# Kernel tuning notes

Measured on AMD Instinct MI355X. Metric: run time of the kernel, lower is better.

The kernel has to match this reference:

```python
import jax, jax.numpy as jnp
import numpy as np
from jax import lax

B, L, NCH, NQ, NL, FW, NCLS = 256, 3000, 4, 8, 2, 128, 5
BN_EPS = 1e-5


def setup_inputs() -> dict:
    key = jax.random.key(0)
    ks = jax.random.split(key, 24)
    rn = lambda k, shape, s=0.05: jax.random.normal(k, shape, jnp.float32) * s
    inp = {}
    inp['x'] = jax.random.normal(ks[0], (B, NCH, L), jnp.float32)
    inp['conv1_w'] = rn(ks[1], (32, NCH, 7)); inp['conv1_b'] = rn(ks[2], (32,))
    inp['bn1_g'] = 1.0 + rn(ks[3], (32,)); inp['bn1_b'] = rn(ks[3], (32,))
    inp['conv2_w'] = rn(ks[4], (64, 32, 7)); inp['conv2_b'] = rn(ks[5], (64,))
    inp['bn2_g'] = 1.0 + rn(ks[6], (64,)); inp['bn2_b'] = rn(ks[6], (64,))
    inp['conv3_w'] = rn(ks[7], (128, 64, 7)); inp['conv3_b'] = rn(ks[8], (128,))
    inp['bn3_g'] = 1.0 + rn(ks[9], (128,)); inp['bn3_b'] = rn(ks[9], (128,))
    inp['conv4_w'] = rn(ks[10], (128, 128, 7)); inp['conv4_b'] = rn(ks[11], (128,))
    inp['bn4_g'] = 1.0 + rn(ks[12], (128,)); inp['bn4_b'] = rn(ks[12], (128,))
    inp['fc_w'] = rn(ks[13], (FW, 128)); inp['fc_b'] = rn(ks[14], (FW,))
    inp['ang_w'] = rn(ks[15], (NQ, FW)); inp['ang_b'] = rn(ks[16], (NQ,))
    # TorchLayer default init: uniform in [0, 2*pi)
    inp['qw'] = jax.random.uniform(ks[17], (NL, NQ, 3), jnp.float32, 0.0, 2.0 * np.pi)
    inp['h1_w'] = rn(ks[18], (64, NQ)); inp['h1_b'] = rn(ks[19], (64,))
    inp['h2_w'] = rn(ks[20], (NCLS, 64)); inp['h2_b'] = rn(ks[21], (NCLS,))
    return inp


def _conv1d(x, w, b):
    y = lax.conv_general_dilated(x, w, (1,), [(3, 3)], dimension_numbers=('NCH', 'OIH', 'NCH'))
    return y + b[None, :, None]


def _bn(x, g, b):  # eval-mode BN: running_mean=0, running_var=1
    inv = 1.0 / np.sqrt(1.0 + BN_EPS)
    return x * (g * inv)[None, :, None] + b[None, :, None]


def _maxpool4(x):
    return lax.reduce_window(x, -jnp.inf, lax.max, (1, 1, 4), (1, 1, 4), 'VALID')


def _apply_1q(state, U, w, batched):
    # state: (B, 2**NQ); wire 0 = most significant bit (PennyLane convention)
    bs = state.shape[0]
    st = state.reshape(bs, 2 ** w, 2, -1)
    if batched:
        new = jnp.einsum('sab,slbr->slar', U, st)
    else:
        new = jnp.einsum('ab,slbr->slar', U, st)
    return new.reshape(bs, -1)


def _apply_cnot(state, c, t):
    bs = state.shape[0]
    q1, q2 = min(c, t), max(c, t)
    s = state.reshape(bs, 2 ** q1, 2, 2 ** (q2 - q1 - 1), 2, -1)
    ci, ti = (2, 4) if c < t else (4, 2)
    c0 = lax.index_in_dim(s, 0, ci, keepdims=True)
    c1 = jnp.flip(lax.index_in_dim(s, 1, ci, keepdims=True), axis=ti)
    return jnp.concatenate([c0, c1], axis=ci).reshape(bs, -1)


def _rot_matrix(phi, th, om):
    # PennyLane Rot(phi, theta, omega) = RZ(omega) RY(theta) RZ(phi)
    cm, sm = jnp.cos(th / 2), jnp.sin(th / 2)
    m00 = jnp.exp(-0.5j * (phi + om)) * cm
    m01 = -jnp.exp(0.5j * (phi - om)) * sm
    m10 = jnp.exp(-0.5j * (phi - om)) * sm
    m11 = jnp.exp(0.5j * (phi + om)) * cm
    return jnp.stack([jnp.stack([m00, m01]), jnp.stack([m10, m11])]).astype(jnp.complex64)


def _qsim(angles, qw):
    bs = angles.shape[0]
    dim = 2 ** NQ
    state = jnp.zeros((bs, dim), jnp.complex64).at[:, 0].set(1.0)
    # AngleEmbedding: RY(angle_w) on each wire (batched matrices)
    c, s = jnp.cos(angles / 2), jnp.sin(angles / 2)
    for w in range(NQ):
        U = jnp.stack([jnp.stack([c[:, w], -s[:, w]], -1),
                       jnp.stack([s[:, w], c[:, w]], -1)], -2).astype(jnp.complex64)
        state = _apply_1q(state, U, w, batched=True)
    # StronglyEntanglingLayers: Rot on each wire, then CNOT ring with range r
    for l in range(NL):
        for w in range(NQ):
            U = _rot_matrix(qw[l, w, 0], qw[l, w, 1], qw[l, w, 2])
            state = _apply_1q(state, U, w, batched=False)
        r = (l % (NQ - 1)) + 1
        for i in range(NQ):
            state = _apply_cnot(state, i, (i + r) % NQ)
    probs = state.real ** 2 + state.imag ** 2
    z = [probs.reshape(bs, 2 ** w, 2, -1)[:, :, 0].sum((1, 2))
         - probs.reshape(bs, 2 ** w, 2, -1)[:, :, 1].sum((1, 2)) for w in range(NQ)]
    return jnp.stack(z, -1)  # (B, NQ)


def reference(x, conv1_w, conv1_b, bn1_g, bn1_b, conv2_w, conv2_b, bn2_g, bn2_b,
              conv3_w, conv3_b, bn3_g, bn3_b, conv4_w, conv4_b, bn4_g, bn4_b,
              fc_w, fc_b, ang_w, ang_b, qw, h1_w, h1_b, h2_w, h2_b):
    h = jax.nn.relu(_bn(_conv1d(x, conv1_w, conv1_b), bn1_g, bn1_b))
    h = jax.nn.relu(_bn(_conv1d(h, conv2_w, conv2_b), bn2_g, bn2_b))
    h = _maxpool4(h)
    h = jax.nn.relu(_bn(_conv1d(h, conv3_w, conv3_b), bn3_g, bn3_b))
    h = _maxpool4(h)
    h = jax.nn.relu(_bn(_conv1d(h, conv4_w, conv4_b), bn4_g, bn4_b))
    h = h.mean(-1)  # AdaptiveAvgPool1d(1) + Flatten -> (B, 128)
    h = jax.nn.relu(h @ fc_w.T + fc_b)  # Dropout is identity in eval
    raw = h @ ang_w.T + ang_b
    angles = np.pi * jnp.tanh(raw)
    q = _qsim(angles, qw)
    h2 = jax.nn.relu(q @ h1_w.T + h1_b)
    return h2 @ h2_w.T + h2_b
```

## Files before the change

kernel.cpp:

```cpp
#include <hip/hip_runtime.h>
#include <hip/hip_bf16.h>

#define BN_INV 0.9999950000375f
#define PI_F   3.14159265358979f

typedef __attribute__((ext_vector_type(8))) short s16x8;
typedef __attribute__((ext_vector_type(4))) float f32x4;
typedef __attribute__((ext_vector_type(4))) unsigned short u16x4;

__device__ inline unsigned short f2bf(float f) {
  union { float f; unsigned u; } v; v.f = f;
  unsigned r = v.u + 0x7fffu + ((v.u >> 16) & 1u);
  return (unsigned short)(r >> 16);
}

__global__ __launch_bounds__(256) void k_pack(
    const float* __restrict__ w1, const float* __restrict__ w2,
    const float* __restrict__ w3, const float* __restrict__ w4,
    const float* __restrict__ fcw,
    unsigned short* __restrict__ w1p, unsigned short* __restrict__ w2p,
    unsigned short* __restrict__ w3p, unsigned short* __restrict__ w4p,
    float* __restrict__ fcwt, float* __restrict__ h4)
{
  int e = blockIdx.x * 256 + threadIdx.x;
  if (e < 2048) {
    int co = e >> 6, k = e & 63, kk = k >> 3, ci = k & 7;
    w1p[e] = (ci < 4 && kk < 7) ? f2bf(w1[co * 28 + ci * 7 + kk]) : (unsigned short)0;
  } else if (e < 16384) {
    int t = e - 2048; int co = t / 224, k = t % 224, kk = k >> 5, ci = k & 31;
    w2p[t] = f2bf(w2[co * 224 + ci * 7 + kk]);
  } else if (e < 73728) {
    int t = e - 16384; int co = t / 448, k = t % 448, kk = k >> 6, ci = k & 63;
    w3p[t] = f2bf(w3[co * 448 + ci * 7 + kk]);
  } else if (e < 188416) {
    int t = e - 73728; int co = t / 896, k = t % 896, kk = k >> 7, ci = k & 127;
    w4p[t] = f2bf(w4[co * 896 + ci * 7 + kk]);
  } else if (e < 221184) {
    h4[e - 188416] = 0.f;
  } else if (e < 237568) {
    int t = e - 221184; int k = t >> 7, o = t & 127;
    fcwt[t] = fcw[o * 128 + k];
  }
}

__global__ __launch_bounds__(256) void k_conv1(
    const float* __restrict__ x, const unsigned short* __restrict__ w1p,
    const float* __restrict__ cb, const float* __restrict__ bng,
    const float* __restrict__ bnb, unsigned short* __restrict__ h1t)
{
  __shared__ __align__(16) char lds[520 * 16 + 4096 + 256];
  float* scs = (float*)(lds + 520 * 16 + 4096);
  const int tid = threadIdx.x;
  const int b = blockIdx.y;
  const int l0 = blockIdx.x * 512;

  for (int r = tid; r < 519; r += 256) {
    int gr = l0 + r - 3;
    s16x8 v;
    if (gr >= 0 && gr < 3000) {
      const float* xr = x + b * 4 * 3000 + gr;
      v[0] = (short)f2bf(xr[0]);
      v[1] = (short)f2bf(xr[3000]);
      v[2] = (short)f2bf(xr[6000]);
      v[3] = (short)f2bf(xr[9000]);
      v[4] = 0; v[5] = 0; v[6] = 0; v[7] = 0;
    } else {
      for (int i = 0; i < 8; ++i) v[i] = 0;
    }
    *(s16x8*)(lds + r * 16) = v;
  }
  {
    int co = tid >> 3, c = tid & 7;
    s16x8 v = *(const s16x8*)(w1p + co * 64 + c * 8);
    *(s16x8*)(lds + 8320 + ((co * 128 + c * 16) ^ ((co & 7) << 4))) = v;
  }
  if (tid < 32) {
    float sc = bng[tid] * BN_INV;
    scs[tid * 2] = sc;
    scs[tid * 2 + 1] = fmaf(cb[tid], sc, bnb[tid]);
  }
  __syncthreads();

  const int w = tid >> 6, l = tid & 63, lr = l & 15, g = l >> 4;
  const int wp = w * 128;
  f32x4 acc[2][8];
  for (int m = 0; m < 2; ++m)
    for (int n = 0; n < 8; ++n)
      for (int i = 0; i < 4; ++i) acc[m][n][i] = 0.f;

  #pragma unroll
  for (int s = 0; s < 2; ++s) {
    s16x8 a[2], bf[8];
    #pragma unroll
    for (int m = 0; m < 2; ++m) {
      int co = m * 16 + lr;
      a[m] = *(const s16x8*)(lds + 8320 + ((co * 128 + s * 64 + g * 16) ^ ((co & 7) << 4)));
    }
    #pragma unroll
    for (int n = 0; n < 8; ++n) {
      int row = wp + n * 16 + lr + s * 4 + g;
      bf[n] = *(const s16x8*)(lds + row * 16);
    }
    #pragma unroll
    for (int m = 0; m < 2; ++m)
      #pragma unroll
      for (int n = 0; n < 8; ++n)
        acc[m][n] = __builtin_amdgcn_mfma_f32_16x16x32_bf16(a[m], bf[n], acc[m][n], 0, 0, 0);
  }

  #pragma unroll
  for (int m = 0; m < 2; ++m) {
    int co0 = m * 16 + g * 4;
    float sc[4], sh[4];
    #pragma unroll
    for (int j = 0; j < 4; ++j) { sc[j] = scs[(co0 + j) * 2]; sh[j] = scs[(co0 + j) * 2 + 1]; }
    #pragma unroll
    for (int n = 0; n < 8; ++n) {
      int gp = l0 + wp + n * 16 + lr;
      if (gp < 3000) {
        u16x4 o;
        #pragma unroll
        for (int j = 0; j < 4; ++j)
          o[j] = f2bf(fmaxf(fmaf(acc[m][n][j], sc[j], sh[j]), 0.f));
        *(u16x4*)(h1t + (b * 3000 + gp) * 32 + co0) = o;
      }
    }
  }
}

__global__ __launch_bounds__(256) void k_conv2(
    const unsigned short* __restrict__ h1t, const unsigned short* __restrict__ w2p,
    const float* __restrict__ cb, const float* __restrict__ bng,
    const float* __restrict__ bnb, unsigned short* __restrict__ h2pt)
{
  __shared__ __align__(16) char lds[46080];
  float* scs = (float*)(lds + 45568);
  const int tid = threadIdx.x, b = blockIdx.y;
  const int l0 = blockIdx.x * 256;

  for (int e = tid; e < 1048; e += 256) {
    int r = e >> 2, c = e & 3;
    int gr = l0 + r - 3;
    s16x8 v;
    if (gr >= 0 && gr < 3000) v = *(const s16x8*)(h1t + (b * 3000 + gr) * 32 + c * 8);
    else for (int i = 0; i < 8; ++i) v[i] = 0;
    *(s16x8*)(lds + ((r * 64 + c * 16) ^ ((r & 7) << 4))) = v;
  }
  for (int e = tid; e < 1792; e += 256) {
    int co = e / 28, c = e % 28;
    s16x8 v = *(const s16x8*)(w2p + co * 224 + c * 8);
    *(s16x8*)(lds + 16896 + ((co * 448 + c * 16) ^ ((co & 7) << 4))) = v;
  }
  if (tid < 64) {
    float sc = bng[tid] * BN_INV;
    scs[tid * 2] = sc;
    scs[tid * 2 + 1] = fmaf(cb[tid], sc, bnb[tid]);
  }
  __syncthreads();

  const int w = tid >> 6, l = tid & 63, lr = l & 15, g = l >> 4;
  const int wp = w * 64;
  f32x4 acc[4][4];
  for (int m = 0; m < 4; ++m)
    for (int n = 0; n < 4; ++n)
      for (int i = 0; i < 4; ++i) acc[m][n][i] = 0.f;

  #pragma unroll
  for (int s = 0; s < 7; ++s) {
    s16x8 xa[4], wb[4];
    #pragma unroll
    for (int m = 0; m < 4; ++m) {
      int row = wp + m * 16 + lr + s;
      xa[m] = *(const s16x8*)(lds + ((row * 64 + g * 16) ^ ((row & 7) << 4)));
    }
    #pragma unroll
    for (int n = 0; n < 4; ++n) {
      int co = n * 16 + lr;
      wb[n] = *(const s16x8*)(lds + 16896 + ((co * 448 + s * 64 + g * 16) ^ ((co & 7) << 4)));
    }
    #pragma unroll
    for (int m = 0; m < 4; ++m)
      #pragma unroll
      for (int n = 0; n < 4; ++n)
        acc[m][n] = __builtin_amdgcn_mfma_f32_16x16x32_bf16(xa[m], wb[n], acc[m][n], 0, 0, 0);
  }

  float sc[4], sh[4];
  #pragma unroll
  for (int n = 0; n < 4; ++n) {
    sc[n] = scs[(n * 16 + lr) * 2];
    sh[n] = scs[(n * 16 + lr) * 2 + 1];
  }
  #pragma unroll
  for (int m = 0; m < 4; ++m) {
    int pp = (l0 + wp + m * 16 + g * 4) >> 2;
    if (pp < 750) {
      unsigned short* orow = h2pt + (b * 750 + pp) * 64 + lr;
      #pragma unroll
      for (int n = 0; n < 4; ++n) {
        float v = fmaxf(fmaxf(acc[m][n][0], acc[m][n][1]),
                        fmaxf(acc[m][n][2], acc[m][n][3]));
        orow[n * 16] = f2bf(fmaxf(fmaf(v, sc[n], sh[n]), 0.f));
      }
    }
  }
}

__global__ __launch_bounds__(256) void k_conv3(
    const unsigned short* __restrict__ h2pt, const unsigned short* __restrict__ w3p,
    const float* __restrict__ cb, const float* __restrict__ bng,
    const float* __restrict__ bnb, unsigned short* __restrict__ h3pt)
{
  __shared__ __align__(16) char lds[75776];
  float* scs = (float*)(lds + 74752);
  const int tid = threadIdx.x, b = blockIdx.y;
  const int l0 = blockIdx.x * 128;

  for (int e = tid; e < 1072; e += 256) {
    int r = e >> 3, c = e & 7;
    int gr = l0 + r - 3;
    s16x8 v;
    if (gr >= 0 && gr < 750) v = *(const s16x8*)(h2pt + (b * 750 + gr) * 64 + c * 8);
    else for (int i = 0; i < 8; ++i) v[i] = 0;
    *(s16x8*)(lds + ((r * 128 + c * 16) ^ ((r & 7) << 4))) = v;
  }
  for (int e = tid; e < 3584; e += 256) {
    int co = e / 28, c = e % 28;
    s16x8 v = *(const s16x8*)(w3p + co * 448 + c * 8);
    *(s16x8*)(lds + 17408 + ((co * 448 + c * 16) ^ ((co & 7) << 4))) = v;
  }
  if (tid < 128) {
    float sc = bng[tid] * BN_INV;
    scs[tid * 2] = sc;
    scs[tid * 2 + 1] = fmaf(cb[tid], sc, bnb[tid]);
  }

  const int lane = tid & 63, wid = tid >> 6;
  const int wr = wid >> 1, wc = wid & 1;
  const int lr = lane & 15, g = lane >> 4;

  f32x4 acc[4][4];
  for (int m = 0; m < 4; ++m)
    for (int n = 0; n < 4; ++n)
      for (int i = 0; i < 4; ++i) acc[m][n][i] = 0.f;

  s16x8 pw[14];
  #pragma unroll
  for (int i = 0; i < 14; ++i) {
    int e = tid + i * 256;
    int co = e / 28, c = e % 28;
    pw[i] = *(const s16x8*)(w3p + co * 448 + 224 + c * 8);
  }
  __syncthreads();

  for (int chunk = 0; chunk < 2; ++chunk) {
    #pragma unroll
    for (int sl = 0; sl < 7; ++sl) {
      int k0 = chunk * 224 + sl * 32;
      int kk = k0 >> 6, cib = k0 & 63;
      s16x8 xa[4], wb[4];
      #pragma unroll
      for (int m = 0; m < 4; ++m) {
        int row = wr * 64 + m * 16 + lr + kk;
        xa[m] = *(const s16x8*)(lds + ((row * 128 + cib * 2 + g * 16) ^ ((row & 7) << 4)));
      }
      #pragma unroll
      for (int n = 0; n < 4; ++n) {
        int co = wc * 64 + n * 16 + lr;
        wb[n] = *(const s16x8*)(lds + 17408 + ((co * 448 + sl * 64 + g * 16) ^ ((co & 7) << 4)));
      }
      #pragma unroll
      for (int m = 0; m < 4; ++m)
        #pragma unroll
        for (int n = 0; n < 4; ++n)
          acc[m][n] = __builtin_amdgcn_mfma_f32_16x16x32_bf16(xa[m], wb[n], acc[m][n], 0, 0, 0);
    }
    if (chunk == 0) {
      __syncthreads();
      #pragma unroll
      for (int i = 0; i < 14; ++i) {
        int e = tid + i * 256;
        int co = e / 28, c = e % 28;
        *(s16x8*)(lds + 17408 + ((co * 448 + c * 16) ^ ((co & 7) << 4))) = pw[i];
      }
      __syncthreads();
    }
  }

  float sc[4], sh[4];
  #pragma unroll
  for (int n = 0; n < 4; ++n) {
    int co = wc * 64 + n * 16 + lr;
    sc[n] = scs[co * 2];
    sh[n] = scs[co * 2 + 1];
  }
  #pragma unroll
  for (int m = 0; m < 4; ++m) {
    int pp = (l0 + wr * 64 + m * 16 + g * 4) >> 2;
    if (pp < 187) {
      unsigned short* orow = h3pt + (b * 187 + pp) * 128;
      #pragma unroll
      for (int n = 0; n < 4; ++n) {
        int co = wc * 64 + n * 16 + lr;
        float v = fmaxf(fmaxf(acc[m][n][0], acc[m][n][1]),
                        fmaxf(acc[m][n][2], acc[m][n][3]));
        orow[co] = f2bf(fmaxf(fmaf(v, sc[n], sh[n]), 0.f));
      }
    }
  }
}

__global__ __launch_bounds__(256) void k_conv4(
    const unsigned short* __restrict__ h3pt, const unsigned short* __restrict__ w4p,
    const float* __restrict__ cb, const float* __restrict__ bng,
    const float* __restrict__ bnb, float* __restrict__ h4)
{
  __shared__ __align__(16) char lds[79872];
  float* scs = (float*)(lds + 79360);
  const int tid = threadIdx.x, b = blockIdx.y, ch = blockIdx.x;
  const int cg0 = ch * 64;

  #pragma unroll
  for (int i = 0; i < 13; ++i) {
    int e = tid + i * 256;
    if (e < 3168) {
      int r = e >> 4, c = e & 15, gr = r - 3;
      s16x8 v;
      if (gr >= 0 && gr < 187) v = *(const s16x8*)(h3pt + (b * 187 + gr) * 128 + c * 8);
      else for (int q = 0; q < 8; ++q) v[q] = 0;
      *(s16x8*)(lds + ((r * 256 + c * 16) ^ ((r & 7) << 4))) = v;
    }
  }
  for (int e = tid; e < 1792; e += 256) {
    int co = e / 28, c = e % 28;
    s16x8 v = *(const s16x8*)(w4p + (cg0 + co) * 896 + c * 8);
    *(s16x8*)(lds + 50688 + ((co * 448 + c * 16) ^ ((co & 7) << 4))) = v;
  }
  if (tid < 64) {
    int co = cg0 + tid;
    float sc = bng[co] * BN_INV;
    scs[tid * 2] = sc;
    scs[tid * 2 + 1] = fmaf(cb[co], sc, bnb[co]);
  }
  __syncthreads();

  const int w = tid >> 6, l = tid & 63, lr = l & 15, g = l >> 4;
  const int wp = w * 48;

  f32x4 acc[3][4];
  for (int m = 0; m < 3; ++m)
    for (int n = 0; n < 4; ++n)
      for (int i = 0; i < 4; ++i) acc[m][n][i] = 0.f;

  for (int chunk = 0; chunk < 4; ++chunk) {
    s16x8 wr[7];
    if (chunk < 3) {
      #pragma unroll
      for (int i = 0; i < 7; ++i) {
        int e = tid + i * 256;
        int co = e / 28, c = e % 28;
        wr[i] = *(const s16x8*)(w4p + (cg0 + co) * 896 + (chunk + 1) * 224 + c * 8);
      }
    }
    #pragma unroll
    for (int sl = 0; sl < 7; ++sl) {
      int k0 = chunk * 224 + sl * 32;
      int kk = k0 >> 7, cib = k0 & 127;
      s16x8 xa[3], wb[4];
      #pragma unroll
      for (int m = 0; m < 3; ++m) {
        int row = wp + m * 16 + lr + kk;
        xa[m] = *(const s16x8*)(lds + ((row * 256 + cib * 2 + g * 16) ^ ((row & 7) << 4)));
      }
      #pragma unroll
      for (int n = 0; n < 4; ++n) {
        int co = n * 16 + lr;
        wb[n] = *(const s16x8*)(lds + 50688 + ((co * 448 + sl * 64 + g * 16) ^ ((co & 7) << 4)));
      }
      #pragma unroll
      for (int m = 0; m < 3; ++m)
        #pragma unroll
        for (int n = 0; n < 4; ++n)
          acc[m][n] = __builtin_amdgcn_mfma_f32_16x16x32_bf16(xa[m], wb[n], acc[m][n], 0, 0, 0);
    }
    __syncthreads();
    if (chunk < 3) {
      #pragma unroll
      for (int i = 0; i < 7; ++i) {
        int e = tid + i * 256;
        int co = e / 28, c = e % 28;
        *(s16x8*)(lds + 50688 + ((co * 448 + c * 16) ^ ((co & 7) << 4))) = wr[i];
      }
    }
    __syncthreads();
  }

  float sc[4], sh[4];
  #pragma unroll
  for (int n = 0; n < 4; ++n) {
    sc[n] = scs[(n * 16 + lr) * 2];
    sh[n] = scs[(n * 16 + lr) * 2 + 1];
  }
  float psum[4] = {0.f, 0.f, 0.f, 0.f};
  #pragma unroll
  for (int m = 0; m < 3; ++m) {
    #pragma unroll
    for (int j = 0; j < 4; ++j) {
      int pos = wp + m * 16 + g * 4 + j;
      if (pos < 187) {
        #pragma unroll
        for (int n = 0; n < 4; ++n)
          psum[n] += fmaxf(fmaf(acc[m][n][j], sc[n], sh[n]), 0.f);
      }
    }
  }
  #pragma unroll
  for (int n = 0; n < 4; ++n) {
    float v = psum[n];
    v += __shfl_xor(v, 16);
    v += __shfl_xor(v, 32);
    if (l < 16)
      atomicAdd(&h4[b * 128 + cg0 + n * 16 + lr], v);
  }
}

__global__ __launch_bounds__(256) void k_umat(
    const float* __restrict__ qw, float2* __restrict__ Ut)
{
  __shared__ float rotm[16][8];
  const int tid = threadIdx.x;
  if (tid < 16) {
    int gq = tid;
    float phi = qw[gq * 3], th = qw[gq * 3 + 1], om = qw[gq * 3 + 2];
    float cm = cosf(0.5f * th), sm = sinf(0.5f * th);
    float ap = 0.5f * (phi + om), bm = 0.5f * (phi - om);
    rotm[gq][0] = cm * cosf(ap);  rotm[gq][1] = -cm * sinf(ap);
    rotm[gq][2] = -sm * cosf(bm); rotm[gq][3] = -sm * sinf(bm);
    rotm[gq][4] = sm * cosf(bm);  rotm[gq][5] = -sm * sinf(bm);
    rotm[gq][6] = cm * cosf(ap);  rotm[gq][7] = cm * sinf(ap);
  }
  __syncthreads();

  const int lane = tid & 63, wid = tid >> 6;
  const int ll = lane & 15;
  const int c = (blockIdx.x * 4 + wid) * 4 + (lane >> 4);

  float2 st[16];
  #pragma unroll
  for (int r = 0; r < 16; ++r) {
    st[r].x = (ll == (c >> 4) && r == (c & 15)) ? 1.f : 0.f;
    st[r].y = 0.f;
  }

#define LOADM(G) \
  float m00x = rotm[G][0], m00y = rotm[G][1], m01x = rotm[G][2], m01y = rotm[G][3], \
        m10x = rotm[G][4], m10y = rotm[G][5], m11x = rotm[G][6], m11y = rotm[G][7];

#define ROT_REG(G, BETA) { LOADM(G) \
  _Pragma("unroll") \
  for (int r = 0; r < 16; ++r) if (!(r & BETA)) { \
    float2 A = st[r], B = st[r + BETA]; \
    st[r].x = m00x*A.x - m00y*A.y + m01x*B.x - m01y*B.y; \
    st[r].y = m00x*A.y + m00y*A.x + m01x*B.y + m01y*B.x; \
    st[r+BETA].x = m10x*A.x - m10y*A.y + m11x*B.x - m11y*B.y; \
    st[r+BETA].y = m10x*A.y + m10y*A.x + m11x*B.y + m11y*B.x; } }

#define ROT_LANE(G, LX) { LOADM(G) \
  _Pragma("unroll") \
  for (int r = 0; r < 16; ++r) { \
    float ox = __shfl_xor(st[r].x, LX); \
    float oy = __shfl_xor(st[r].y, LX); \
    bool hi = (lane & LX) != 0; \
    float a0x = hi ? ox : st[r].x, a0y = hi ? oy : st[r].y; \
    float a1x = hi ? st[r].x : ox, a1y = hi ? st[r].y : oy; \
    float cx = hi ? m10x : m00x, cy = hi ? m10y : m00y; \
    float dx = hi ? m11x : m01x, dy = hi ? m11y : m01y; \
    st[r].x = cx*a0x - cy*a0y + dx*a1x - dy*a1y; \
    st[r].y = cx*a0y + cy*a0x + dx*a1y + dy*a1x; } }
// ... 15 lines not shown
    float2 A = st[r], B = st[r + BT]; \
    st[r].x = cc ? B.x : A.x;  st[r].y = cc ? B.y : A.y; \
    st[r+BT].x = cc ? A.x : B.x;  st[r+BT].y = cc ? A.y : B.y; } }

#define CNOT_LL(LXC, LXT) { bool cc = (lane & LXC) != 0; \
  _Pragma("unroll") \
  for (int r = 0; r < 16; ++r) { \
    float ox = __shfl_xor(st[r].x, LXT); \
    float oy = __shfl_xor(st[r].y, LXT); \
    if (cc) { st[r].x = ox; st[r].y = oy; } } }

  ROT_LANE(0, 8) ROT_LANE(1, 4) ROT_LANE(2, 2) ROT_LANE(3, 1)
  ROT_REG(4, 8)  ROT_REG(5, 4)  ROT_REG(6, 2)  ROT_REG(7, 1)
  CNOT_LL(8, 4) CNOT_LL(4, 2) CNOT_LL(2, 1) CNOT_LR(1, 8)
  CNOT_RR(8, 4) CNOT_RR(4, 2) CNOT_RR(2, 1) CNOT_RL(1, 8)
  ROT_LANE(8, 8) ROT_LANE(9, 4) ROT_LANE(10, 2) ROT_LANE(11, 1)
  ROT_REG(12, 8) ROT_REG(13, 4) ROT_REG(14, 2)  ROT_REG(15, 1)
  CNOT_LL(8, 2) CNOT_LL(4, 1) CNOT_LR(2, 8) CNOT_LR(1, 4)
  CNOT_RR(8, 2) CNOT_RR(4, 1) CNOT_RL(2, 8) CNOT_RL(1, 4)

#undef LOADM
#undef ROT_REG
#undef ROT_LANE
#undef CNOT_RR
#undef CNOT_RL
#undef CNOT_LR
#undef CNOT_LL

  float2* uc = Ut + c * 256 + ll * 16;
  #pragma unroll
  for (int r = 0; r < 16; r += 2) {
    float4 v = make_float4(st[r].x, st[r].y, st[r + 1].x, st[r + 1].y);
    *(float4*)(uc + r) = v;
  }
}

__global__ __launch_bounds__(256) void k_head2(
    const float* __restrict__ h4, const float* __restrict__ fc_wt,
    const float* __restrict__ fc_b, const float* __restrict__ ang_w,
    const float* __restrict__ ang_b, const float* __restrict__ h1_w,
    const float* __restrict__ h1_b, const float* __restrict__ h2_w,
    const float* __restrict__ h2_b, const float2* __restrict__ Ut,
    float* __restrict__ out)
{
  __shared__ float h4v[512];
  __shared__ float fvec[512];
  __shared__ float rcs[64];
  __shared__ float4 e4[256];
  __shared__ float4 parr[256];
  __shared__ float zsum[32];
  __shared__ float hh[256];

  const int tid = threadIdx.x;
  const int b0 = blockIdx.x * 4;

  #pragma unroll
  for (int q = 0; q < 2; ++q) {
    int task = tid + q * 256;
    h4v[task] = h4[(b0 + (task >> 7)) * 128 + (task & 127)] * (1.0f / 187.0f);
  }
  __syncthreads();

  #pragma unroll
  for (int q = 0; q < 2; ++q) {
    int task = tid + q * 256;
    int bb = task >> 7, o = task & 127;
// ... 94 lines not shown
  const float* x    = (const float*)d_in[0];
  const float* c1w  = (const float*)d_in[1];
  const float* c1b  = (const float*)d_in[2];
  const float* b1g  = (const float*)d_in[3];
  const float* b1b  = (const float*)d_in[4];
  const float* c2w  = (const float*)d_in[5];
  const float* c2b  = (const float*)d_in[6];
  const float* b2g  = (const float*)d_in[7];
  const float* b2b  = (const float*)d_in[8];
  const float* c3w  = (const float*)d_in[9];
  const float* c3b  = (const float*)d_in[10];
  const float* b3g  = (const float*)d_in[11];
  const float* b3b  = (const float*)d_in[12];
  const float* c4w  = (const float*)d_in[13];
  const float* c4b  = (const float*)d_in[14];
  const float* b4g  = (const float*)d_in[15];
  const float* b4b  = (const float*)d_in[16];
  const float* fcw  = (const float*)d_in[17];
  const float* fcb  = (const float*)d_in[18];
  const float* angw = (const float*)d_in[19];
  const float* angb = (const float*)d_in[20];
  const float* qw   = (const float*)d_in[21];
  const float* h1w  = (const float*)d_in[22];
  const float* h1b  = (const float*)d_in[23];
  const float* h2w  = (const float*)d_in[24];
  const float* h2b  = (const float*)d_in[25];

  char* wsb = (char*)d_ws;
  unsigned short* w1p  = (unsigned short*)(wsb + 0);
  unsigned short* w2p  = (unsigned short*)(wsb + 4096);
  unsigned short* w3p  = (unsigned short*)(wsb + 32768);
  unsigned short* w4p  = (unsigned short*)(wsb + 147456);
  float*          h4   = (float*)(wsb + 393216);
  unsigned short* h1t  = (unsigned short*)(wsb + 1048576);
  unsigned short* h2pt = (unsigned short*)(wsb + 52428800);
  unsigned short* h3pt = (unsigned short*)(wsb + 79691776);
  float2*         Ut   = (float2*)(wsb + 100663296);
  float*          fcwt = (float*)(wsb + 101187584);

  k_pack<<<dim3(928), 256, 0, stream>>>(c1w, c2w, c3w, c4w, fcw,
                                        w1p, w2p, w3p, w4p, fcwt, h4);
  k_umat<<<dim3(16), 256, 0, stream>>>(qw, Ut);
  k_conv1<<<dim3(6, 256),  256, 0, stream>>>(x, w1p, c1b, b1g, b1b, h1t);
  k_conv2<<<dim3(12, 256), 256, 0, stream>>>(h1t, w2p, c2b, b2g, b2b, h2pt);
  k_conv3<<<dim3(6, 256),  256, 0, stream>>>(h2pt, w3p, c3b, b3g, b3b, h3pt);
  k_conv4<<<dim3(2, 256),  256, 0, stream>>>(h3pt, w4p, c4b, b4g, b4b, h4);
  k_head2<<<dim3(64), 256, 0, stream>>>(h4, fcwt, fcb, angw, angb,
                                        h1w, h1b, h2w, h2b, Ut, (float*)d_out);
}
```

Measured before the change: 248.0 us.

## Fuse conv1 into conv2 via LDS halo tile and merge pack with umat

Computes conv1 inside the conv2 kernel: each block loads a haloed strip of the input, builds the conv1 activations for that strip in LDS, then runs conv2 and the maxpool from there. This removes the global write and read of the large bf16 h1t intermediate and one kernel launch. Weight packing and unitary construction also share one launch now, split by block index. The cost is a small amount of recomputed conv1 work on the halo rows and more LDS per block, which may lower occupancy.

```diff
diff --git a/kernel.cpp b/kernel.cpp
--- a/kernel.cpp
+++ b/kernel.cpp
@@ -14,421 +14,42 @@
   return (unsigned short)(r >> 16);
 }
 
-__global__ __launch_bounds__(256) void k_pack(
+__global__ __launch_bounds__(256) void k_packumat(
     const float* __restrict__ w1, const float* __restrict__ w2,
     const float* __restrict__ w3, const float* __restrict__ w4,
-    const float* __restrict__ fcw,
+    const float* __restrict__ fcw, const float* __restrict__ qw,
     unsigned short* __restrict__ w1p, unsigned short* __restrict__ w2p,
     unsigned short* __restrict__ w3p, unsigned short* __restrict__ w4p,
-    float* __restrict__ fcwt, float* __restrict__ h4)
-{
-  int e = blockIdx.x * 256 + threadIdx.x;
-  if (e < 2048) {
-    int co = e >> 6, k = e & 63, kk = k >> 3, ci = k & 7;
-    w1p[e] = (ci < 4 && kk < 7) ? f2bf(w1[co * 28 + ci * 7 + kk]) : (unsigned short)0;
-  } else if (e < 16384) {
-    int t = e - 2048; int co = t / 224, k = t % 224, kk = k >> 5, ci = k & 31;
-    w2p[t] = f2bf(w2[co * 224 + ci * 7 + kk]);
-  } else if (e < 73728) {
-    int t = e - 16384; int co = t / 448, k = t % 448, kk = k >> 6, ci = k & 63;
-    w3p[t] = f2bf(w3[co * 448 + ci * 7 + kk]);
-  } else if (e < 188416) {
-    int t = e - 73728; int co = t / 896, k = t % 896, kk = k >> 7, ci = k & 127;
-    w4p[t] = f2bf(w4[co * 896 + ci * 7 + kk]);
-  } else if (e < 221184) {
-    h4[e - 188416] = 0.f;
-  } else if (e < 237568) {
-    int t = e - 221184; int k = t >> 7, o = t & 127;
-    fcwt[t] = fcw[o * 128 + k];
-  }
-}
-
-__global__ __launch_bounds__(256) void k_conv1(
-    const float* __restrict__ x, const unsigned short* __restrict__ w1p,
-    const float* __restrict__ cb, const float* __restrict__ bng,
-    const float* __restrict__ bnb, unsigned short* __restrict__ h1t)
-{
-  __shared__ __align__(16) char lds[520 * 16 + 4096 + 256];
-  float* scs = (float*)(lds + 520 * 16 + 4096);
-  const int tid = threadIdx.x;
-  const int b = blockIdx.y;
-  const int l0 = blockIdx.x * 512;
-
-  for (int r = tid; r < 519; r += 256) {
-    int gr = l0 + r - 3;
-    s16x8 v;
-    if (gr >= 0 && gr < 3000) {
-      const float* xr = x + b * 4 * 3000 + gr;
-      v[0] = (short)f2bf(xr[0]);
-      v[1] = (short)f2bf(xr[3000]);
-      v[2] = (short)f2bf(xr[6000]);
-      v[3] = (short)f2bf(xr[9000]);
-      v[4] = 0; v[5] = 0; v[6] = 0; v[7] = 0;
-    } else {
-      for (int i = 0; i < 8; ++i) v[i] = 0;
-    }
-    *(s16x8*)(lds + r * 16) = v;
-  }
-  {
-    int co = tid >> 3, c = tid & 7;
-    s16x8 v = *(const s16x8*)(w1p + co * 64 + c * 8);
-    *(s16x8*)(lds + 8320 + ((co * 128 + c * 16) ^ ((co & 7) << 4))) = v;
-  }
-  if (tid < 32) {
-    float sc = bng[tid] * BN_INV;
-    scs[tid * 2] = sc;
-    scs[tid * 2 + 1] = fmaf(cb[tid], sc, bnb[tid]);
-  }
-  __syncthreads();
-
-  const int w = tid >> 6, l = tid & 63, lr = l & 15, g = l >> 4;
-  const int wp = w * 128;
-  f32x4 acc[2][8];
-  for (int m = 0; m < 2; ++m)
-    for (int n = 0; n < 8; ++n)
-      for (int i = 0; i < 4; ++i) acc[m][n][i] = 0.f;
-
-  #pragma unroll
-  for (int s = 0; s < 2; ++s) {
-    s16x8 a[2], bf[8];
-    #pragma unroll
-    for (int m = 0; m < 2; ++m) {
-      int co = m * 16 + lr;
-      a[m] = *(const s16x8*)(lds + 8320 + ((co * 128 + s * 64 + g * 16) ^ ((co & 7) << 4)));
-    }
-    #pragma unroll
-    for (int n = 0; n < 8; ++n) {
-      int row = wp + n * 16 + lr + s * 4 + g;
-      bf[n] = *(const s16x8*)(lds + row * 16);
-    }
-    #pragma unroll
-    for (int m = 0; m < 2; ++m)
-      #pragma unroll
-      for (int n = 0; n < 8; ++n)
-        acc[m][n] = __builtin_amdgcn_mfma_f32_16x16x32_bf16(a[m], bf[n], acc[m][n], 0, 0, 0);
-  }
-
-  #pragma unroll
-  for (int m = 0; m < 2; ++m) {
-    int co0 = m * 16 + g * 4;
-    float sc[4], sh[4];
-    #pragma unroll
-    for (int j = 0; j < 4; ++j) { sc[j] = scs[(co0 + j) * 2]; sh[j] = scs[(co0 + j) * 2 + 1]; }
-    #pragma unroll
-    for (int n = 0; n < 8; ++n) {
-      int gp = l0 + wp + n * 16 + lr;
-      if (gp < 3000) {
-        u16x4 o;
-        #pragma unroll
-        for (int j = 0; j < 4; ++j)
-          o[j] = f2bf(fmaxf(fmaf(acc[m][n][j], sc[j], sh[j]), 0.f));
-        *(u16x4*)(h1t + (b * 3000 + gp) * 32 + co0) = o;
-      }
-    }
-  }
-}
-
-__global__ __launch_bounds__(256) void k_conv2(
-    const unsigned short* __restrict__ h1t, const unsigned short* __restrict__ w2p,
-    const float* __restrict__ cb, const float* __restrict__ bng,
-    const float* __restrict__ bnb, unsigned short* __restrict__ h2pt)
-{
-  __shared__ __align__(16) char lds[46080];
-  float* scs = (float*)(lds + 45568);
-  const int tid = threadIdx.x, b = blockIdx.y;
-  const int l0 = blockIdx.x * 256;
-
-  for (int e = tid; e < 1048; e += 256) {
-    int r = e >> 2, c = e & 3;
-    int gr = l0 + r - 3;
-    s16x8 v;
-    if (gr >= 0 && gr < 3000) v = *(const s16x8*)(h1t + (b * 3000 + gr) * 32 + c * 8);
-    else for (int i = 0; i < 8; ++i) v[i] = 0;
-    *(s16x8*)(lds + ((r * 64 + c * 16) ^ ((r & 7) << 4))) = v;
-  }
-  for (int e = tid; e < 1792; e += 256) {
-    int co = e / 28, c = e % 28;
-    s16x8 v = *(const s16x8*)(w2p + co * 224 + c * 8);
-    *(s16x8*)(lds + 16896 + ((co * 448 + c * 16) ^ ((co & 7) << 4))) = v;
-  }
-  if (tid < 64) {
-    float sc = bng[tid] * BN_INV;
-    scs[tid * 2] = sc;
-    scs[tid * 2 + 1] = fmaf(cb[tid], sc, bnb[tid]);
-  }
-  __syncthreads();
-
-  const int w = tid >> 6, l = tid & 63, lr = l & 15, g = l >> 4;
-  const int wp = w * 64;
-  f32x4 acc[4][4];
-  for (int m = 0; m < 4; ++m)
-    for (int n = 0; n < 4; ++n)
-      for (int i = 0; i < 4; ++i) acc[m][n][i] = 0.f;
-
-  #pragma unroll
-  for (int s = 0; s < 7; ++s) {
-    s16x8 xa[4], wb[4];
-    #pragma unroll
-    for (int m = 0; m < 4; ++m) {
-      int row = wp + m * 16 + lr + s;
-      xa[m] = *(const s16x8*)(lds + ((row * 64 + g * 16) ^ ((row & 7) << 4)));
-    }
-    #pragma unroll
-    for (int n = 0; n < 4; ++n) {
-      int co = n * 16 + lr;
-      wb[n] = *(const s16x8*)(lds + 16896 + ((co * 448 + s * 64 + g * 16) ^ ((co & 7) << 4)));
-    }
-    #pragma unroll
-    for (int m = 0; m < 4; ++m)
-      #pragma unroll
-      for (int n = 0; n < 4; ++n)
-        acc[m][n] = __builtin_amdgcn_mfma_f32_16x16x32_bf16(xa[m], wb[n], acc[m][n], 0, 0, 0);
-  }
-
-  float sc[4], sh[4];
-  #pragma unroll
-  for (int n = 0; n < 4; ++n) {
-    sc[n] = scs[(n * 16 + lr) * 2];
-    sh[n] = scs[(n * 16 + lr) * 2 + 1];
-  }
-  #pragma unroll
-  for (int m = 0; m < 4; ++m) {
-    int pp = (l0 + wp + m * 16 + g * 4) >> 2;
-    if (pp < 750) {
-      unsigned short* orow = h2pt + (b * 750 + pp) * 64 + lr;
-      #pragma unroll
-      for (int n = 0; n < 4; ++n) {
-        float v = fmaxf(fmaxf(acc[m][n][0], acc[m][n][1]),
-                        fmaxf(acc[m][n][2], acc[m][n][3]));
-        orow[n * 16] = f2bf(fmaxf(fmaf(v, sc[n], sh[n]), 0.f));
-      }
-    }
-  }
-}
-
-__global__ __launch_bounds__(256) void k_conv3(
-    const unsigned short* __restrict__ h2pt, const unsigned short* __restrict__ w3p,
-    const float* __restrict__ cb, const float* __restrict__ bng,
-    const float* __restrict__ bnb, unsigned short* __restrict__ h3pt)
-{
-  __shared__ __align__(16) char lds[75776];
-  float* scs = (float*)(lds + 74752);
-  const int tid = threadIdx.x, b = blockIdx.y;
-  const int l0 = blockIdx.x * 128;
-
-  for (int e = tid; e < 1072; e += 256) {
-    int r = e >> 3, c = e & 7;
-    int gr = l0 + r - 3;
-    s16x8 v;
-    if (gr >= 0 && gr < 750) v = *(const s16x8*)(h2pt + (b * 750 + gr) * 64 + c * 8);
-    else for (int i = 0; i < 8; ++i) v[i] = 0;
-    *(s16x8*)(lds + ((r * 128 + c * 16) ^ ((r & 7) << 4))) = v;
-  }
-  for (int e = tid; e < 3584; e += 256) {
-    int co = e / 28, c = e % 28;
-    s16x8 v = *(const s16x8*)(w3p + co * 448 + c * 8);
-    *(s16x8*)(lds + 17408 + ((co * 448 + c * 16) ^ ((co & 7) << 4))) = v;
-  }
-  if (tid < 128) {
-    float sc = bng[tid] * BN_INV;
-    scs[tid * 2] = sc;
-    scs[tid * 2 + 1] = fmaf(cb[tid], sc, bnb[tid]);
-  }
-
-  const int lane = tid & 63, wid = tid >> 6;
-  const int wr = wid >> 1, wc = wid & 1;
-  const int lr = lane & 15, g = lane >> 4;
-
-  f32x4 acc[4][4];
-  for (int m = 0; m < 4; ++m)
-    for (int n = 0; n < 4; ++n)
-      for (int i = 0; i < 4; ++i) acc[m][n][i] = 0.f;
-
-  s16x8 pw[14];
-  #pragma unroll
-  for (int i = 0; i < 14; ++i) {
-    int e = tid + i * 256;
-    int co = e / 28, c = e % 28;
-    pw[i] = *(const s16x8*)(w3p + co * 448 + 224 + c * 8);
-  }
-  __syncthreads();
-
-  for (int chunk = 0; chunk < 2; ++chunk) {
-    #pragma unroll
-    for (int sl = 0; sl < 7; ++sl) {
-      int k0 = chunk * 224 + sl * 32;
-      int kk = k0 >> 6, cib = k0 & 63;
-      s16x8 xa[4], wb[4];
-      #pragma unroll
-      for (int m = 0; m < 4; ++m) {
-        int row = wr * 64 + m * 16 + lr + kk;
-        xa[m] = *(const s16x8*)(lds + ((row * 128 + cib * 2 + g * 16) ^ ((row & 7) << 4)));
-      }
-      #pragma unroll
-      for (int n = 0; n < 4; ++n) {
-        int co = wc * 64 + n * 16 + lr;
-        wb[n] = *(const s16x8*)(lds + 17408 + ((co * 448 + sl * 64 + g * 16) ^ ((co & 7) << 4)));
-      }
-      #pragma unroll
-      for (int m = 0; m < 4; ++m)
-        #pragma unroll
-        for (int n = 0; n < 4; ++n)
-          acc[m][n] = __builtin_amdgcn_mfma_f32_16x16x32_bf16(xa[m], wb[n], acc[m][n], 0, 0, 0);
-    }
-    if (chunk == 0) {
-      __syncthreads();
-      #pragma unroll
-      for (int i = 0; i < 14; ++i) {
-        int e = tid + i * 256;
-        int co = e / 28, c = e % 28;
-        *(s16x8*)(lds + 17408 + ((co * 448 + c * 16) ^ ((co & 7) << 4))) = pw[i];
-      }
-      __syncthreads();
-    }
-  }
-
-  float sc[4], sh[4];
-  #pragma unroll
-  for (int n = 0; n < 4; ++n) {
-    int co = wc * 64 + n * 16 + lr;
-    sc[n] = scs[co * 2];
-    sh[n] = scs[co * 2 + 1];
-  }
-  #pragma unroll
-  for (int m = 0; m < 4; ++m) {
-    int pp = (l0 + wr * 64 + m * 16 + g * 4) >> 2;
-    if (pp < 187) {
-      unsigned short* orow = h3pt + (b * 187 + pp) * 128;
-      #pragma unroll
-      for (int n = 0; n < 4; ++n) {
-        int co = wc * 64 + n * 16 + lr;
-        float v = fmaxf(fmaxf(acc[m][n][0], acc[m][n][1]),
-                        fmaxf(acc[m][n][2], acc[m][n][3]));
-        orow[co] = f2bf(fmaxf(fmaf(v, sc[n], sh[n]), 0.f));
-      }
-    }
-  }
-}
-
-__global__ __launch_bounds__(256) void k_conv4(
-    const unsigned short* __restrict__ h3pt, const unsigned short* __restrict__ w4p,
-    const float* __restrict__ cb, const float* __restrict__ bng,
-    const float* __restrict__ bnb, float* __restrict__ h4)
-{
-  __shared__ __align__(16) char lds[79872];
-  float* scs = (float*)(lds + 79360);
-  const int tid = threadIdx.x, b = blockIdx.y, ch = blockIdx.x;
-  const int cg0 = ch * 64;
-
-  #pragma unroll
-  for (int i = 0; i < 13; ++i) {
-    int e = tid + i * 256;
-    if (e < 3168) {
-      int r = e >> 4, c = e & 15, gr = r - 3;
-      s16x8 v;
-      if (gr >= 0 && gr < 187) v = *(const s16x8*)(h3pt + (b * 187 + gr) * 128 + c * 8);
-      else for (int q = 0; q < 8; ++q) v[q] = 0;
-      *(s16x8*)(lds + ((r * 256 + c * 16) ^ ((r & 7) << 4))) = v;
-    }
-  }
-  for (int e = tid; e < 1792; e += 256) {
-    int co = e / 28, c = e % 28;
-    s16x8 v = *(const s16x8*)(w4p + (cg0 + co) * 896 + c * 8);
-    *(s16x8*)(lds + 50688 + ((co * 448 + c * 16) ^ ((co & 7) << 4))) = v;
-  }
-  if (tid < 64) {
-    int co = cg0 + tid;
-    float sc = bng[co] * BN_INV;
-    scs[tid * 2] = sc;
-    scs[tid * 2 + 1] = fmaf(cb[co], sc, bnb[co]);
-  }
-  __syncthreads();
-
-  const int w = tid >> 6, l = tid & 63, lr = l & 15, g = l >> 4;
-  const int wp = w * 48;
-
-  f32x4 acc[3][4];
-  for (int m = 0; m < 3; ++m)
-    for (int n = 0; n < 4; ++n)
-      for (int i = 0; i < 4; ++i) acc[m][n][i] = 0.f;
-
-  for (int chunk = 0; chunk < 4; ++chunk) {
-    s16x8 wr[7];
-    if (chunk < 3) {
-      #pragma unroll
-      for (int i = 0; i < 7; ++i) {
-        int e = tid + i * 256;
-        int co = e / 28, c = e % 28;
-        wr[i] = *(const s16x8*)(w4p + (cg0 + co) * 896 + (chunk + 1) * 224 + c * 8);
-      }
-    }
-    #pragma unroll
-    for (int sl = 0; sl < 7; ++sl) {
-      int k0 = chunk * 224 + sl * 32;
-      int kk = k0 >> 7, cib = k0 & 127;
-      s16x8 xa[3], wb[4];
-      #pragma unroll
-      for (int m = 0; m < 3; ++m) {
-        int row = wp + m * 16 + lr + kk;
-        xa[m] = *(const s16x8*)(lds + ((row * 256 + cib * 2 + g * 16) ^ ((row & 7) << 4)));
-      }
-      #pragma unroll
-      for (int n = 0; n < 4; ++n) {
-        int co = n * 16 + lr;
-        wb[n] = *(const s16x8*)(lds + 50688 + ((co * 448 + sl * 64 + g * 16) ^ ((co & 7) << 4)));
-      }
-      #pragma unroll
-      for (int m = 0; m < 3; ++m)
-        #pragma unroll
-        for (int n = 0; n < 4; ++n)
-          acc[m][n] = __builtin_amdgcn_mfma_f32_16x16x32_bf16(xa[m], wb[n], acc[m][n], 0, 0, 0);
-    }
-    __syncthreads();
-    if (chunk < 3) {
-      #pragma unroll
-      for (int i = 0; i < 7; ++i) {
-        int e = tid + i * 256;
-        int co = e / 28, c = e % 28;
-        *(s16x8*)(lds + 50688 + ((co * 448 + c * 16) ^ ((co & 7) << 4))) = wr[i];
-      }
-    }
-    __syncthreads();
-  }
-
-  float sc[4], sh[4];
-  #pragma unroll
-  for (int n = 0; n < 4; ++n) {
-    sc[n] = scs[(n * 16 + lr) * 2];
-    sh[n] = scs[(n * 16 + lr) * 2 + 1];
-  }
-  float psum[4] = {0.f, 0.f, 0.f, 0.f};
-  #pragma unroll
-  for (int m = 0; m < 3; ++m) {
-    #pragma unroll
-    for (int j = 0; j < 4; ++j) {
-      int pos = wp + m * 16 + g * 4 + j;
-      if (pos < 187) {
-        #pragma unroll
-        for (int n = 0; n < 4; ++n)
-          psum[n] += fmaxf(fmaf(acc[m][n][j], sc[n], sh[n]), 0.f);
-      }
-    }
-  }
-  #pragma unroll
-  for (int n = 0; n < 4; ++n) {
-    float v = psum[n];
-    v += __shfl_xor(v, 16);
-    v += __shfl_xor(v, 32);
-    if (l < 16)
-      atomicAdd(&h4[b * 128 + cg0 + n * 16 + lr], v);
-  }
-}
-
-__global__ __launch_bounds__(256) void k_umat(
-    const float* __restrict__ qw, float2* __restrict__ Ut)
+    float* __restrict__ fcwt, float* __restrict__ h4,
+    float2* __restrict__ Ut)
 {
   __shared__ float rotm[16][8];
   const int tid = threadIdx.x;
+
+  if (blockIdx.x < 928) {
+    int e = blockIdx.x * 256 + tid;
+    if (e < 2048) {
+      int co = e >> 6, k = e & 63, kk = k >> 3, ci = k & 7;
+      w1p[e] = (ci < 4 && kk < 7) ? f2bf(w1[co * 28 + ci * 7 + kk]) : (unsigned short)0;
+    } else if (e < 16384) {
+      int t = e - 2048; int co = t / 224, k = t % 224, kk = k >> 5, ci = k & 31;
+      w2p[t] = f2bf(w2[co * 224 + ci * 7 + kk]);
+    } else if (e < 73728) {
+      int t = e - 16384; int co = t / 448, k = t % 448, kk = k >> 6, ci = k & 63;
+      w3p[t] = f2bf(w3[co * 448 + ci * 7 + kk]);
+    } else if (e < 188416) {
+      int t = e - 73728; int co = t / 896, k = t % 896, kk = k >> 7, ci = k & 127;
+      w4p[t] = f2bf(w4[co * 896 + ci * 7 + kk]);
+    } else if (e < 221184) {
+      h4[e - 188416] = 0.f;
+    } else if (e < 237568) {
+      int t = e - 221184; int k = t >> 7, o = t & 127;
+      fcwt[t] = fcw[o * 128 + k];
+    }
+    return;
+  }
+
+  const int bx = blockIdx.x - 928;
   if (tid < 16) {
     int gq = tid;
     float phi = qw[gq * 3], th = qw[gq * 3 + 1], om = qw[gq * 3 + 2];
@@ -443,7 +64,7 @@
 
   const int lane = tid & 63, wid = tid >> 6;
   const int ll = lane & 15;
-  const int c = (blockIdx.x * 4 + wid) * 4 + (lane >> 4);
+  const int c = (bx * 4 + wid) * 4 + (lane >> 4);
 
   float2 st[16];
   #pragma unroll
@@ -525,6 +146,361 @@
   for (int r = 0; r < 16; r += 2) {
     float4 v = make_float4(st[r].x, st[r].y, st[r + 1].x, st[r + 1].y);
     *(float4*)(uc + r) = v;
+  }
+}
+
+__global__ __launch_bounds__(256) void k_conv12(
+    const float* __restrict__ x, const unsigned short* __restrict__ w1p,
+    const unsigned short* __restrict__ w2p,
+    const float* __restrict__ c1b, const float* __restrict__ b1g,
+    const float* __restrict__ b1b,
+    const float* __restrict__ c2b, const float* __restrict__ b2g,
+    const float* __restrict__ b2b,
+    unsigned short* __restrict__ h2pt)
+{
+  __shared__ __align__(16) char lds[50816];
+  const int XR = 0;
+  const int H1 = 4480;
+  const int W2 = 21376;
+  float* s1 = (float*)(lds + 50048);
+  float* s2 = (float*)(lds + 50304);
+
+  const int tid = threadIdx.x, b = blockIdx.y;
+  const int l0 = blockIdx.x * 256;
+
+  for (int r = tid; r < 280; r += 256) {
+    int gp = l0 - 6 + r;
+    s16x8 v;
+    for (int i = 0; i < 8; ++i) v[i] = 0;
+    if (r < 268 && gp >= 0 && gp < 3000) {
+      const float* xr = x + b * 4 * 3000 + gp;
+      v[0] = (short)f2bf(xr[0]);
+      v[1] = (short)f2bf(xr[3000]);
+      v[2] = (short)f2bf(xr[6000]);
+      v[3] = (short)f2bf(xr[9000]);
+    }
+    *(s16x8*)(lds + XR + r * 16) = v;
+  }
+  for (int e = tid; e < 1792; e += 256) {
+    int co = e / 28, cc = e % 28;
+    s16x8 v = *(const s16x8*)(w2p + co * 224 + cc * 8);
+    *(s16x8*)(lds + W2 + ((co * 448 + cc * 16) ^ ((co & 7) << 4))) = v;
+  }
+  if (tid < 32) {
+    float sc = b1g[tid] * BN_INV;
+    s1[tid * 2] = sc;
+    s1[tid * 2 + 1] = fmaf(c1b[tid], sc, b1b[tid]);
+  }
+  if (tid < 64) {
+    float sc = b2g[tid] * BN_INV;
+    s2[tid * 2] = sc;
+    s2[tid * 2 + 1] = fmaf(c2b[tid], sc, b2b[tid]);
+  }
+  __syncthreads();
+
+  const int w = tid >> 6, lane = tid & 63, lr = lane & 15, g = lane >> 4;
+
+  {
+    s16x8 a1[2][2];
+    #pragma unroll
+    for (int m = 0; m < 2; ++m)
+      #pragma unroll
+      for (int s = 0; s < 2; ++s)
+        a1[m][s] = *(const s16x8*)(w1p + (m * 16 + lr) * 64 + s * 32 + g * 8);
+
+    #pragma unroll
+    for (int t = 0; t < 5; ++t) {
+      int tile = w + t * 4;
+      if (tile >= 17) break;
+      int p0 = tile * 16;
+      f32x4 acc[2];
+      for (int m = 0; m < 2; ++m)
+        for (int i = 0; i < 4; ++i) acc[m][i] = 0.f;
+      #pragma unroll
+      for (int s = 0; s < 2; ++s) {
+        s16x8 bf = *(const s16x8*)(lds + XR + (p0 + lr + s * 4 + g) * 16);
+        acc[0] = __builtin_amdgcn_mfma_f32_16x16x32_bf16(a1[0][s], bf, acc[0], 0, 0, 0);
+        acc[1] = __builtin_amdgcn_mfma_f32_16x16x32_bf16(a1[1][s], bf, acc[1], 0, 0, 0);
+      }
+      int r2 = p0 + lr;
+      if (r2 < 262) {
+        #pragma unroll
+        for (int m = 0; m < 2; ++m) {
+          int co0 = m * 16 + g * 4;
+          u16x4 o;
+          #pragma unroll
+          for (int j = 0; j < 4; ++j)
+            o[j] = f2bf(fmaxf(fmaf(acc[m][j], s1[(co0 + j) * 2], s1[(co0 + j) * 2 + 1]), 0.f));
+          int byte = ((r2 * 64 + (co0 >> 3) * 16) ^ ((r2 & 7) << 4)) + (co0 & 7) * 2;
+          *(u16x4*)(lds + H1 + byte) = o;
+        }
+      }
+    }
+  }
+  __syncthreads();
+
+  const int wp = w * 64;
+  f32x4 acc[4][4];
+  for (int m = 0; m < 4; ++m)
+    for (int n = 0; n < 4; ++n)
+      for (int i = 0; i < 4; ++i) acc[m][n][i] = 0.f;
+
+  #pragma unroll
+  for (int s = 0; s < 7; ++s) {
+    s16x8 xa[4], wb[4];
+    #pragma unroll
+    for (int m = 0; m < 4; ++m) {
+      int row = wp + m * 16 + lr + s;
+      xa[m] = *(const s16x8*)(lds + H1 + ((row * 64 + g * 16) ^ ((row & 7) << 4)));
+    }
+    #pragma unroll
+    for (int n = 0; n < 4; ++n) {
+      int co = n * 16 + lr;
+      wb[n] = *(const s16x8*)(lds + W2 + ((co * 448 + s * 64 + g * 16) ^ ((co & 7) << 4)));
+    }
+    #pragma unroll
+    for (int m = 0; m < 4; ++m)
+      #pragma unroll
+      for (int n = 0; n < 4; ++n)
+        acc[m][n] = __builtin_amdgcn_mfma_f32_16x16x32_bf16(xa[m], wb[n], acc[m][n], 0, 0, 0);
+  }
+
+  float sc[4], sh[4];
+  #pragma unroll
+  for (int n = 0; n < 4; ++n) {
+    sc[n] = s2[(n * 16 + lr) * 2];
+    sh[n] = s2[(n * 16 + lr) * 2 + 1];
+  }
+  #pragma unroll
+  for (int m = 0; m < 4; ++m) {
+    int pp = (l0 + wp + m * 16 + g * 4) >> 2;
+    if (pp < 750) {
+      unsigned short* orow = h2pt + (b * 750 + pp) * 64 + lr;
+      #pragma unroll
+      for (int n = 0; n < 4; ++n) {
+        float v = fmaxf(fmaxf(acc[m][n][0], acc[m][n][1]),
+                        fmaxf(acc[m][n][2], acc[m][n][3]));
+        orow[n * 16] = f2bf(fmaxf(fmaf(v, sc[n], sh[n]), 0.f));
+      }
+    }
+  }
+}
+
+__global__ __launch_bounds__(256) void k_conv3(
+    const unsigned short* __restrict__ h2pt, const unsigned short* __restrict__ w3p,
+    const float* __restrict__ cb, const float* __restrict__ bng,
+    const float* __restrict__ bnb, unsigned short* __restrict__ h3pt)
+{
+  __shared__ __align__(16) char lds[75776];
+  float* scs = (float*)(lds + 74752);
+  const int tid = threadIdx.x, b = blockIdx.y;
+  const int l0 = blockIdx.x * 128;
+
+  for (int e = tid; e < 1072; e += 256) {
+    int r = e >> 3, c = e & 7;
+    int gr = l0 + r - 3;
+    s16x8 v;
+    if (gr >= 0 && gr < 750) v = *(const s16x8*)(h2pt + (b * 750 + gr) * 64 + c * 8);
+    else for (int i = 0; i < 8; ++i) v[i] = 0;
+    *(s16x8*)(lds + ((r * 128 + c * 16) ^ ((r & 7) << 4))) = v;
+  }
+  for (int e = tid; e < 3584; e += 256) {
+    int co = e / 28, c = e % 28;
+    s16x8 v = *(const s16x8*)(w3p + co * 448 + c * 8);
+    *(s16x8*)(lds + 17408 + ((co * 448 + c * 16) ^ ((co & 7) << 4))) = v;
+  }
+  if (tid < 128) {
+    float sc = bng[tid] * BN_INV;
+    scs[tid * 2] = sc;
+    scs[tid * 2 + 1] = fmaf(cb[tid], sc, bnb[tid]);
+  }
+
+  const int lane = tid & 63, wid = tid >> 6;
+  const int wr = wid >> 1, wc = wid & 1;
+  const int lr = lane & 15, g = lane >> 4;
+
+  f32x4 acc[4][4];
+  for (int m = 0; m < 4; ++m)
+    for (int n = 0; n < 4; ++n)
+      for (int i = 0; i < 4; ++i) acc[m][n][i] = 0.f;
+
+  s16x8 pw[14];
+  #pragma unroll
+  for (int i = 0; i < 14; ++i) {
+    int e = tid + i * 256;
+    int co = e / 28, c = e % 28;
+    pw[i] = *(const s16x8*)(w3p + co * 448 + 224 + c * 8);
+  }
+  __syncthreads();
+
+  for (int chunk = 0; chunk < 2; ++chunk) {
+    #pragma unroll
+    for (int sl = 0; sl < 7; ++sl) {
+      int k0 = chunk * 224 + sl * 32;
+      int kk = k0 >> 6, cib = k0 & 63;
+      s16x8 xa[4], wb[4];
+      #pragma unroll
+      for (int m = 0; m < 4; ++m) {
+        int row = wr * 64 + m * 16 + lr + kk;
+        xa[m] = *(const s16x8*)(lds + ((row * 128 + cib * 2 + g * 16) ^ ((row & 7) << 4)));
+      }
+      #pragma unroll
+      for (int n = 0; n < 4; ++n) {
+        int co = wc * 64 + n * 16 + lr;
+        wb[n] = *(const s16x8*)(lds + 17408 + ((co * 448 + sl * 64 + g * 16) ^ ((co & 7) << 4)));
+      }
+      #pragma unroll
+      for (int m = 0; m < 4; ++m)
+        #pragma unroll
+        for (int n = 0; n < 4; ++n)
+          acc[m][n] = __builtin_amdgcn_mfma_f32_16x16x32_bf16(xa[m], wb[n], acc[m][n], 0, 0, 0);
+    }
+    if (chunk == 0) {
+      __syncthreads();
+      #pragma unroll
+      for (int i = 0; i < 14; ++i) {
+        int e = tid + i * 256;
+        int co = e / 28, c = e % 28;
+        *(s16x8*)(lds + 17408 + ((co * 448 + c * 16) ^ ((co & 7) << 4))) = pw[i];
+      }
+      __syncthreads();
+    }
+  }
+
+  float sc[4], sh[4];
+  #pragma unroll
+  for (int n = 0; n < 4; ++n) {
+    int co = wc * 64 + n * 16 + lr;
+    sc[n] = scs[co * 2];
+    sh[n] = scs[co * 2 + 1];
+  }
+  #pragma unroll
+  for (int m = 0; m < 4; ++m) {
+    int pp = (l0 + wr * 64 + m * 16 + g * 4) >> 2;
+    if (pp < 187) {
+      unsigned short* orow = h3pt + (b * 187 + pp) * 128;
+      #pragma unroll
+      for (int n = 0; n < 4; ++n) {
+        int co = wc * 64 + n * 16 + lr;
+        float v = fmaxf(fmaxf(acc[m][n][0], acc[m][n][1]),
+                        fmaxf(acc[m][n][2], acc[m][n][3]));
+        orow[co] = f2bf(fmaxf(fmaf(v, sc[n], sh[n]), 0.f));
+      }
+    }
+  }
+}
+
+__global__ __launch_bounds__(256) void k_conv4(
+    const unsigned short* __restrict__ h3pt, const unsigned short* __restrict__ w4p,
+    const float* __restrict__ cb, const float* __restrict__ bng,
+    const float* __restrict__ bnb, float* __restrict__ h4)
+{
+  __shared__ __align__(16) char lds[79872];
+  float* scs = (float*)(lds + 79360);
+  const int tid = threadIdx.x, b = blockIdx.y, ch = blockIdx.x;
+  const int cg0 = ch * 64;
+
+  #pragma unroll
+  for (int i = 0; i < 13; ++i) {
+    int e = tid + i * 256;
+    if (e < 3168) {
+      int r = e >> 4, c = e & 15, gr = r - 3;
+      s16x8 v;
+      if (gr >= 0 && gr < 187) v = *(const s16x8*)(h3pt + (b * 187 + gr) * 128 + c * 8);
+      else for (int q = 0; q < 8; ++q) v[q] = 0;
+      *(s16x8*)(lds + ((r * 256 + c * 16) ^ ((r & 7) << 4))) = v;
+    }
+  }
+  for (int e = tid; e < 1792; e += 256) {
+    int co = e / 28, c = e % 28;
+    s16x8 v = *(const s16x8*)(w4p + (cg0 + co) * 896 + c * 8);
+    *(s16x8*)(lds + 50688 + ((co * 448 + c * 16) ^ ((co & 7) << 4))) = v;
+  }
+  if (tid < 64) {
+    int co = cg0 + tid;
+    float sc = bng[co] * BN_INV;
+    scs[tid * 2] = sc;
+    scs[tid * 2 + 1] = fmaf(cb[co], sc, bnb[co]);
+  }
+  __syncthreads();
+
+  const int w = tid >> 6, l = tid & 63, lr = l & 15, g = l >> 4;
+  const int wp = w * 48;
+
+  f32x4 acc[3][4];
+  for (int m = 0; m < 3; ++m)
+    for (int n = 0; n < 4; ++n)
+      for (int i = 0; i < 4; ++i) acc[m][n][i] = 0.f;
+
+  for (int chunk = 0; chunk < 4; ++chunk) {
+    s16x8 wr[7];
+    if (chunk < 3) {
+      #pragma unroll
+      for (int i = 0; i < 7; ++i) {
+        int e = tid + i * 256;
+        int co = e / 28, c = e % 28;
+        wr[i] = *(const s16x8*)(w4p + (cg0 + co) * 896 + (chunk + 1) * 224 + c * 8);
+      }
+    }
+    #pragma unroll
+    for (int sl = 0; sl < 7; ++sl) {
+      int k0 = chunk * 224 + sl * 32;
+      int kk = k0 >> 7, cib = k0 & 127;
+      s16x8 xa[3], wb[4];
+      #pragma unroll
+      for (int m = 0; m < 3; ++m) {
+        int row = wp + m * 16 + lr + kk;
+        xa[m] = *(const s16x8*)(lds + ((row * 256 + cib * 2 + g * 16) ^ ((row & 7) << 4)));
+      }
+      #pragma unroll
+      for (int n = 0; n < 4; ++n) {
+        int co = n * 16 + lr;
+        wb[n] = *(const s16x8*)(lds + 50688 + ((co * 448 + sl * 64 + g * 16) ^ ((co & 7) << 4)));
+      }
+      #pragma unroll
+      for (int m = 0; m < 3; ++m)
+        #pragma unroll
+        for (int n = 0; n < 4; ++n)
+          acc[m][n] = __builtin_amdgcn_mfma_f32_16x16x32_bf16(xa[m], wb[n], acc[m][n], 0, 0, 0);
+    }
+    __syncthreads();
+    if (chunk < 3) {
+      #pragma unroll
+      for (int i = 0; i < 7; ++i) {
+        int e = tid + i * 256;
+        int co = e / 28, c = e % 28;
+        *(s16x8*)(lds + 50688 + ((co * 448 + c * 16) ^ ((co & 7) << 4))) = wr[i];
+      }
+    }
+    __syncthreads();
+  }
+
+  float sc[4], sh[4];
+  #pragma unroll
+  for (int n = 0; n < 4; ++n) {
+    sc[n] = scs[(n * 16 + lr) * 2];
+    sh[n] = scs[(n * 16 + lr) * 2 + 1];
+  }
+  float psum[4] = {0.f, 0.f, 0.f, 0.f};
+  #pragma unroll
+  for (int m = 0; m < 3; ++m) {
+    #pragma unroll
+    for (int j = 0; j < 4; ++j) {
+      int pos = wp + m * 16 + g * 4 + j;
+      if (pos < 187) {
+        #pragma unroll
+        for (int n = 0; n < 4; ++n)
+          psum[n] += fmaxf(fmaf(acc[m][n][j], sc[n], sh[n]), 0.f);
+      }
+    }
+  }
+  #pragma unroll
+  for (int n = 0; n < 4; ++n) {
+    float v = psum[n];
+    v += __shfl_xor(v, 16);
+    v += __shfl_xor(v, 32);
+    if (l < 16)
+      atomicAdd(&h4[b * 128 + cg0 + n * 16 + lr], v);
   }
 }
 
@@ -685,19 +661,17 @@
   unsigned short* w3p  = (unsigned short*)(wsb + 32768);
   unsigned short* w4p  = (unsigned short*)(wsb + 147456);
   float*          h4   = (float*)(wsb + 393216);
-  unsigned short* h1t  = (unsigned short*)(wsb + 1048576);
   unsigned short* h2pt = (unsigned short*)(wsb + 52428800);
   unsigned short* h3pt = (unsigned short*)(wsb + 79691776);
   float2*         Ut   = (float2*)(wsb + 100663296);
   float*          fcwt = (float*)(wsb + 101187584);
 
-  k_pack<<<dim3(928), 256, 0, stream>>>(c1w, c2w, c3w, c4w, fcw,
-                                        w1p, w2p, w3p, w4p, fcwt, h4);
-  k_umat<<<dim3(16), 256, 0, stream>>>(qw, Ut);
-  k_conv1<<<dim3(6, 256),  256, 0, stream>>>(x, w1p, c1b, b1g, b1b, h1t);
-  k_conv2<<<dim3(12, 256), 256, 0, stream>>>(h1t, w2p, c2b, b2g, b2b, h2pt);
-  k_conv3<<<dim3(6, 256),  256, 0, stream>>>(h2pt, w3p, c3b, b3g, b3b, h3pt);
-  k_conv4<<<dim3(2, 256),  256, 0, stream>>>(h3pt, w4p, c4b, b4g, b4b, h4);
+  k_packumat<<<dim3(944), 256, 0, stream>>>(c1w, c2w, c3w, c4w, fcw, qw,
+                                            w1p, w2p, w3p, w4p, fcwt, h4, Ut);
+  k_conv12<<<dim3(12, 256), 256, 0, stream>>>(x, w1p, w2p, c1b, b1g, b1b,
+                                              c2b, b2g, b2b, h2pt);
+  k_conv3<<<dim3(6, 256), 256, 0, stream>>>(h2pt, w3p, c3b, b3g, b3b, h3pt);
+  k_conv4<<<dim3(2, 256), 256, 0, stream>>>(h3pt, w4p, c4b, b4g, b4b, h4);
   k_head2<<<dim3(64), 256, 0, stream>>>(h4, fcwt, fcb, angw, angb,
                                         h1w, h1b, h2w, h2b, Ut, (float*)d_out);
 }
```

Result: faster. 237.1 us (-4.4%).
